# Kernel tuning notes

Hardware: AMD Instinct MI355X
Metric: run time of the kernel (lower is better)

## Reference

```python
import jax, jax.numpy as jnp
import numpy as np

B, S, HID = 1, 2048, 4096
NH, NKV, D = 32, 8, 128
SCALE = D ** -0.5


def _rope_tables(seq_len, head_dim, base=10000.0):
    inv_freq = 1.0 / (base ** (jnp.arange(0, head_dim, 2, dtype=jnp.float32) / head_dim))
    freqs = jnp.arange(seq_len, dtype=jnp.float32)[:, None] * inv_freq[None, :]  # [S, D/2]
    emb = jnp.concatenate([freqs, freqs], axis=-1)  # [S, D]
    return jnp.cos(emb), jnp.sin(emb)


def _rotate_half(x):
    half = x.shape[-1] // 2
    return jnp.concatenate([-x[..., half:], x[..., :half]], axis=-1)


def setup_inputs() -> dict:
    key = jax.random.key(0)
    ks = jax.random.split(key, 5)
    hidden = jax.random.normal(ks[0], (B, S, HID), dtype=jnp.float32)
    cos, sin = _rope_tables(S, D)
    # additive causal mask: 0 on/below diagonal, large negative above
    neg = jnp.full((S, S), -1e9, dtype=jnp.float32)
    causal_mask = jnp.triu(neg, k=1)[None, None]  # [1,1,S,S]
    std_in = HID ** -0.5
    Wq = jax.random.normal(ks[1], (HID, NH * D), dtype=jnp.float32) * std_in
    Wk = jax.random.normal(ks[2], (HID, NKV * D), dtype=jnp.float32) * std_in
    Wv = jax.random.normal(ks[3], (HID, NKV * D), dtype=jnp.float32) * std_in
    Wo = jax.random.normal(ks[4], (NH * D, HID), dtype=jnp.float32) * ((NH * D) ** -0.5)
    return {"hidden": hidden, "cos": cos, "sin": sin, "causal_mask": causal_mask,
            "Wq": Wq, "Wk": Wk, "Wv": Wv, "Wo": Wo}


def reference(hidden, cos, sin, causal_mask, Wq, Wk, Wv, Wo):
    b, s, _ = hidden.shape
    q = (hidden @ Wq).reshape(b, s, NH, D).transpose(0, 2, 1, 3)    # [B,H,S,D]
    k = (hidden @ Wk).reshape(b, s, NKV, D).transpose(0, 2, 1, 3)   # [B,Hkv,S,D]
    v = (hidden @ Wv).reshape(b, s, NKV, D).transpose(0, 2, 1, 3)
    c = cos[None, None]  # [1,1,S,D]
    sn = sin[None, None]
    q = q * c + _rotate_half(q) * sn
    k = k * c + _rotate_half(k) * sn
    group = NH // NKV
    if group > 1:
        k = jnp.repeat(k, group, axis=1)  # [B,H,S,D]
        v = jnp.repeat(v, group, axis=1)
    scores = jnp.einsum('bhsd,bhtd->bhst', q, k) * SCALE + causal_mask
    attn = jax.nn.softmax(scores.astype(jnp.float32), axis=-1).astype(v.dtype)
    ctx = jnp.einsum('bhst,bhtd->bhsd', attn, v)
    ctx = ctx.transpose(0, 2, 1, 3).reshape(b, s, NH * D)
    return ctx @ Wo
```

## Files before the change

### kernel.cpp

```cpp
#include <hip/hip_runtime.h>
#include <hip/hip_bf16.h>
#include <cstdint>
#include <cstddef>

typedef __attribute__((ext_vector_type(8))) short bf16x8;
typedef __attribute__((ext_vector_type(4))) float f32x4;
typedef __attribute__((ext_vector_type(4))) unsigned int u32x4;

__device__ __forceinline__ unsigned short f2bf(float f) {
  __hip_bfloat16 h = __float2bfloat16(f);
  return *reinterpret_cast<unsigned short*>(&h);
}
__device__ __forceinline__ float bf2f(unsigned short u) {
  __hip_bfloat16 h = *reinterpret_cast<__hip_bfloat16*>(&u);
  return __bfloat162float(h);
}

typedef const __attribute__((address_space(1))) void gas_void;
typedef __attribute__((address_space(3))) void las_void;
__device__ __forceinline__ void gload_lds16(const void* g, void* l) {
  __builtin_amdgcn_global_load_lds((gas_void*)g, (las_void*)l, 16, 0, 0);
}

template <int N>
__device__ __forceinline__ void waitcnt_vm() {
  asm volatile("s_waitcnt vmcnt(%0)" :: "i"(N) : "memory");
}
#define LGKM0 { asm volatile("s_waitcnt lgkmcnt(0)" ::: "memory"); \
                __builtin_amdgcn_sched_barrier(0); }

#define S_LEN 2048
#define HID 4096
#define NH 32
#define NKV 8
#define HD 128
#define NQKV 6144
static const float ATT_SCALE = 0.08838834764831845f;


__global__ void prep_kernel(const float* __restrict__ hidden, short* __restrict__ hid_bf,
                            const float* __restrict__ Wq, const float* __restrict__ Wk,
                            const float* __restrict__ Wv, const float* __restrict__ Wo,
                            short* __restrict__ Wcat, short* __restrict__ WoT) {
  __shared__ float tile[64][33];
  const int bid = blockIdx.x;
  const int t = threadIdx.x;
  if (bid >= 20480) {
    int i = ((bid - 20480) * 256 + t) * 8;
    f32x4 a = *(const f32x4*)(hidden + i);
    f32x4 b = *(const f32x4*)(hidden + i + 4);
    unsigned short o[8];
#pragma unroll
    for (int k = 0; k < 4; ++k) { o[k] = f2bf(a[k]); o[4 + k] = f2bf(b[k]); }
    *(u32x4*)(hid_bf + i) = *(const u32x4*)o;
    return;
  }
  const float* src; short* dst; int N, loc;
  if (bid < 8192)       { src = Wq; dst = Wcat;                      N = 4096; loc = bid; }
  else if (bid < 10240) { src = Wk; dst = Wcat + (size_t)4096 * HID; N = 1024; loc = bid - 8192; }
  else if (bid < 12288) { src = Wv; dst = Wcat + (size_t)5120 * HID; N = 1024; loc = bid - 10240; }
  else                  { src = Wo; dst = WoT;                       N = 4096; loc = bid - 12288; }
  const int kb = (loc & 63) * 64, nb = (loc >> 6) * 32;
  {
    int kr = t >> 3, c4 = (t & 7) * 4;
#pragma unroll
    for (int i = 0; i < 2; ++i) {
      int k = kr + i * 32;
      f32x4 v = *(const f32x4*)(src + (size_t)(kb + k) * N + nb + c4);
      tile[k][c4] = v[0]; tile[k][c4 + 1] = v[1];
      tile[k][c4 + 2] = v[2]; tile[k][c4 + 3] = v[3];
    }
  }
  __syncthreads();
  int n = t >> 3, k0 = (t & 7) * 8;
  unsigned short o[8];
#pragma unroll
  for (int i = 0; i < 8; ++i) o[i] = f2bf(tile[k0 + i][n]);
  *(u32x4*)(dst + (size_t)(nb + n) * HID + kb + k0) = *(const u32x4*)o;
}


#define READ_A(MHL) { \
    const short* As_ = lds + (kt & 1) * BUF; \
    _Pragma("unroll") for (int m = 0; m < MHALF; ++m) \
    _Pragma("unroll") for (int kk = 0; kk < 2; ++kk) { \
      int row = (MHL) * (BM / 2) + wr * MSTEP + m * 16 + r; \
      int c = kk * 4 + g; \
      af[m][kk] = *(const bf16x8*)(As_ + row * 64 + ((c ^ (row & 7)) * 8)); \
    } }
#define READ_B(NHL) { \
    const short* Bs_ = lds + (kt & 1) * BUF + BM * 64; \
    _Pragma("unroll") for (int n = 0; n < NHALF; ++n) \
    _Pragma("unroll") for (int kk = 0; kk < 2; ++kk) { \
      int row = (NHL) * (BN / 2) + wc * NSTEP + n * 16 + r; \
      int c = kk * 4 + g; \
      bf[n][kk] = *(const bf16x8*)(Bs_ + row * 64 + ((c ^ (row & 7)) * 8)); \
    } }
#define MFMA_QUAD(MHL, NHL) { \
    __builtin_amdgcn_s_setprio(1); \
    _Pragma("unroll") for (int m = 0; m < MHALF; ++m) \
    _Pragma("unroll") for (int n = 0; n < NHALF; ++n) \
    _Pragma("unroll") for (int kk = 0; kk < 2; ++kk) \
      acc[(MHL)*MHALF + m][(NHL)*NHALF + n] = __builtin_amdgcn_mfma_f32_16x16x32_bf16( \
          af[m][kk], bf[n][kk], acc[(MHL)*MHALF + m][(NHL)*NHALF + n], 0, 0, 0); \
    __builtin_amdgcn_s_setprio(0); }

template <int MODE, int BM, int BN, int WM, int WN>
__global__ __launch_bounds__(WM * WN * 64, 2) void gemm8p_kernel(
    const short* __restrict__ A, const short* __restrict__ Bt,
    int M, int N, int K,
    float* __restrict__ Cf, short* __restrict__ qb_,
    short* __restrict__ kb_, short* __restrict__ vb_) {
  constexpr int NT = WM * WN * 64;
  constexpr int M_FR = BM / (WM * 16);
  constexpr int N_FR = BN / (WN * 16);
  constexpr int MHALF = M_FR / 2;
  constexpr int NHALF = N_FR / 2;
  constexpr int MSTEP = BM / (2 * WM);
  constexpr int NSTEP = BN / (2 * WN);
  constexpr int LA = (BM / 2) * 8 / NT;
  constexpr int LB = (BN / 2) * 8 / NT;
  constexpr int BUF = (BM + BN) * 64;

  __shared__ short lds[2 * BUF];

  const int tid = threadIdx.x, wid = tid >> 6, lane = tid & 63;
  const int wr = wid / WN, wc = wid % WN;
  const int r = lane & 15, g = lane >> 4;
  const int brow = blockIdx.y * BM, bcol = blockIdx.x * BN;
  const int T = K >> 6;

  f32x4 acc[M_FR][N_FR] = {};
  bf16x8 af[MHALF][2], bf[NHALF][2];

  auto stage_rgn = [&](int kt, int rgn) {
    short* buf = lds + (kt & 1) * BUF;
    if (rgn == 0 || rgn == 3) {
      const int mh = (rgn == 3);
      short* dst = buf + mh * (BM / 2) * 64;
      const short* src = A + (size_t)(brow + mh * (BM / 2)) * K + kt * 64;
#pragma unroll
      for (int i = 0; i < LA; ++i) {
        int slot = i * NT + tid;
        int row = slot >> 3, c2 = slot & 7;
        gload_lds16(src + (size_t)row * K + ((c2 ^ (row & 7)) * 8), dst + slot * 8);
      }
    } else {
      const int nh = (rgn == 2);
      short* dst = buf + BM * 64 + nh * (BN / 2) * 64;
      const short* src = Bt + (size_t)(bcol + nh * (BN / 2)) * K + kt * 64;
#pragma unroll
      for (int i = 0; i < LB; ++i) {
        int slot = i * NT + tid;
        int row = slot >> 3, c2 = slot & 7;
        gload_lds16(src + (size_t)row * K + ((c2 ^ (row & 7)) * 8), dst + slot * 8);
      }
    }
  };

  stage_rgn(0, 0); stage_rgn(0, 1); stage_rgn(0, 2); stage_rgn(0, 3);

  for (int kt = 0; kt < T; ++kt) {
    const bool nl = (kt + 1 < T);
    waitcnt_vm<0>();
    __builtin_amdgcn_s_barrier();
    __builtin_amdgcn_sched_barrier(0);
    READ_A(0); READ_B(0);
    if (nl) { stage_rgn(kt + 1, 0); stage_rgn(kt + 1, 1);
              stage_rgn(kt + 1, 2); stage_rgn(kt + 1, 3); }
    LGKM0;
    MFMA_QUAD(0, 0);
    READ_B(1);
    LGKM0;
    MFMA_QUAD(0, 1);
    READ_A(1);
    LGKM0;
    MFMA_QUAD(1, 1);
    READ_B(0);
    LGKM0;
    MFMA_QUAD(1, 0);
  }

  if (MODE == 0) {
#pragma unroll
    for (int fm = 0; fm < M_FR; ++fm)
#pragma unroll
      for (int fn = 0; fn < N_FR; ++fn)
#pragma unroll
        for (int j = 0; j < 4; ++j) {
          int row = brow + (fm / MHALF) * (BM / 2) + wr * MSTEP + (fm % MHALF) * 16 + g * 4 + j;
          int col = bcol + (fn / NHALF) * (BN / 2) + wc * NSTEP + (fn % NHALF) * 16 + r;
          Cf[(size_t)row * N + col] = acc[fm][fn][j];
        }
  } else {
#pragma unroll
    for (int fn = 0; fn < N_FR; ++fn) {
      const int cb = bcol + (fn / NHALF) * (BN / 2) + wc * NSTEP + (fn % NHALF) * 16;
      if (cb < 4096) {
        unsigned short* dst = (unsigned short*)qb_ + (size_t)(cb >> 7) * S_LEN * HD;
        const int d0 = cb & 127;
#pragma unroll
        for (int fm = 0; fm < M_FR; ++fm)
#pragma unroll
          for (int j = 0; j < 4; ++j) {
            int row = brow + (fm / MHALF) * (BM / 2) + wr * MSTEP + (fm % MHALF) * 16 + g * 4 + j;
            dst[(size_t)row * HD + d0 + r] = f2bf(acc[fm][fn][j]);
          }
      } else if (cb < 5120) {
        char* base = (char*)kb_ + ((size_t)((cb - 4096) >> 7) << 19);
        const int d = cb & 127;
#pragma unroll
        for (int fm = 0; fm < M_FR; ++fm)
#pragma unroll
          for (int j = 0; j < 4; ++j) {
            int row = brow + (fm / MHALF) * (BM / 2) + wr * MSTEP + (fm % MHALF) * 16 + g * 4 + j;
            int dd = d + r;
            int krow = row & 63;
            size_t off = ((size_t)(row >> 6) << 14) +
                         ((((krow << 8) + ((dd >> 3) << 4)) ^ ((krow & 7) << 4)) + ((dd & 7) << 1));
            *(unsigned short*)(base + off) = f2bf(acc[fm][fn][j]);
          }
      } else {
        char* base = (char*)vb_ + ((size_t)((cb - 5120) >> 7) << 19);
        const int d = cb & 127;
#pragma unroll
        for (int fm = 0; fm < M_FR; ++fm)
#pragma unroll
          for (int j = 0; j < 4; ++j) {
            int row = brow + (fm / MHALF) * (BM / 2) + wr * MSTEP + (fm % MHALF) * 16 + g * 4 + j;
            int dd = d + r;
            int sl = row & 63;
            size_t off = ((size_t)(row >> 6) << 14) +
                         ((((dd << 7) + ((sl >> 3) << 4)) ^ ((dd & 7) << 4)) + ((sl & 7) << 1));
            *(unsigned short*)(base + off) = f2bf(acc[fm][fn][j]);
          }
      }
    }
  }
}

__global__ void rope_kernel(short* __restrict__ qbuf, short* __restrict__ kbuf,
                            const float* __restrict__ cosT, const float* __restrict__ sinT) {
  int idx = blockIdx.x * 256 + threadIdx.x;
  const int total = (NH + NKV) * S_LEN * 64;
  if (idx >= total) return;
  int d = idx & 63;
  int rowi = idx >> 6;
  int s;
  unsigned short *p1, *p2;
  if (rowi < NH * S_LEN) {
    unsigned short* base = (unsigned short*)qbuf + (size_t)rowi * HD;
    s = rowi & (S_LEN - 1);
    p1 = base + d; p2 = base + d + 64;
  } else {
    int kr = rowi - NH * S_LEN;
    int kvh = kr >> 11; s = kr & (S_LEN - 1);
    char* base = (char*)kbuf + ((size_t)kvh << 19) + ((size_t)(s >> 6) << 14);
    int krow = s & 63, swz = (krow & 7) << 4;
    int dd = d + 64;
    p1 = (unsigned short*)(base + ((((krow << 8) + ((d >> 3) << 4)) ^ swz) + ((d & 7) << 1)));
    p2 = (unsigned short*)(base + ((((krow << 8) + ((dd >> 3) << 4)) ^ swz) + ((dd & 7) << 1)));
  }
  float x1 = bf2f(*p1);
  float x2 = bf2f(*p2);
  float c1 = cosT[s * HD + d], s1 = sinT[s * HD + d];
  *p1 = f2bf(x1 * c1 - x2 * s1);
  *p2 = f2bf(x2 * c1 + x1 * s1);
}

__global__ __launch_bounds__(512, 2) void attn_kernel(const short* __restrict__ qb_,
                                                      const short* __restrict__ kb_,
                                                      const short* __restrict__ vb_,
                                                      short* __restrict__ ctx) {
  const int bid = blockIdx.x;
  const int kvh = bid & 7;
  const int idx = bid >> 3;
  const int h = kvh * 4 + (idx & 3);
  const int slot = idx >> 2;
  const int tid = threadIdx.x, wid = tid >> 6, lane = tid & 63;
  const int r = lane & 15, g = lane >> 4;

  __shared__ short Ks[2][64 * 128];
  __shared__ short Vts[2][128 * 64];
  __shared__ short Ps[8][16 * 64];

  const int qb2s[2] = { slot, 15 - slot };
  const int nt0 = 2 * qb2s[0] + 2;
  const int T = 34;

  const char* kvbase_k = (const char*)kb_ + ((size_t)kvh << 19);
  const char* kvbase_v = (const char*)vb_ + ((size_t)kvh << 19);

  auto stage = [&](int tg, int b) {
    int kvt = (tg < nt0) ? tg : (tg - nt0);
    const char* kt = kvbase_k + ((size_t)kvt << 14);
    const char* vt = kvbase_v + ((size_t)kvt << 14);
#pragma unroll
    for (int i = 0; i < 2; ++i) {
      int ch = i * 8 + wid;
      gload_lds16(kt + ch * 1024 + lane * 16, (char*)&Ks[b][0] + ch * 1024);
      gload_lds16(vt + ch * 1024 + lane * 16, (char*)&Vts[b][0] + ch * 1024);
    }
  };

  stage(0, 0);
  int cur = 0, tglob = 0;

  for (int sec = 0; sec < 2; ++sec) {
    const int qb2 = qb2s[sec];
    const int nt = 2 * qb2 + 2;
    const int rowbase = qb2 * 128 + wid * 16;

    const unsigned short* qptr =
        (const unsigned short*)qb_ + ((size_t)h * S_LEN + rowbase) * HD;
    bf16x8 qf[4];
#pragma unroll
    for (int s4 = 0; s4 < 4; ++s4)
      qf[s4] = *(const bf16x8*)(qptr + (size_t)r * HD + s4 * 32 + g * 8);

    f32x4 oacc[8] = {};
    float m_run[4], l_run[4];
#pragma unroll
    for (int j = 0; j < 4; ++j) { m_run[j] = -1e30f; l_run[j] = 0.f; }

    for (int kvt = 0; kvt < nt; ++kvt, ++tglob) {
      __syncthreads();
      if (tglob + 1 < T) stage(tglob + 1, cur ^ 1);

      const char* Kc = (const char*)&Ks[cur][0];
      const char* Vc = (const char*)&Vts[cur][0];

      f32x4 sv[4] = {};
      __builtin_amdgcn_s_setprio(1);
#pragma unroll
      for (int n = 0; n < 4; ++n) {
        int krow = n * 16 + r;
        int swz = (krow & 7) << 4;
#pragma unroll
        for (int s4 = 0; s4 < 4; ++s4) {
          bf16x8 kf = *(const bf16x8*)(Kc + ((krow * 256 + s4 * 64 + g * 16) ^ swz));
          sv[n] = __builtin_amdgcn_mfma_f32_16x16x32_bf16(qf[s4], kf, sv[n], 0, 0, 0);
        }
      }
      __builtin_amdgcn_s_setprio(0);

      if (kvt * 64 + 63 > rowbase) {
#pragma unroll
        for (int n = 0; n < 4; ++n)
#pragma unroll
          for (int j = 0; j < 4; ++j) {
            int colg = kvt * 64 + n * 16 + r;
            int rowg = rowbase + g * 4 + j;
            sv[n][j] = (colg <= rowg) ? sv[n][j] * ATT_SCALE : -1e30f;
          }
      } else {
#pragma unroll
        for (int n = 0; n < 4; ++n)
#pragma unroll
          for (int j = 0; j < 4; ++j) sv[n][j] *= ATT_SCALE;
      }

      float pmax[4];
#pragma unroll
      for (int j = 0; j < 4; ++j)
        pmax[j] = fmaxf(fmaxf(sv[0][j], sv[1][j]), fmaxf(sv[2][j], sv[3][j]));
#pragma unroll
      for (int msk = 1; msk <= 8; msk <<= 1)
#pragma unroll
        for (int j = 0; j < 4; ++j) pmax[j] = fmaxf(pmax[j], __shfl_xor(pmax[j], msk));

      float sf[4], rsum[4];
#pragma unroll
      for (int j = 0; j < 4; ++j) {
        float mn = fmaxf(m_run[j], pmax[j]);
        sf[j] = __expf(m_run[j] - mn);
        m_run[j] = mn;
        rsum[j] = 0.f;
      }
#pragma unroll
      for (int n = 0; n < 4; ++n)
#pragma unroll
        for (int j = 0; j < 4; ++j) {
          float p = __expf(sv[n][j] - m_run[j]);
          sv[n][j] = p;
          rsum[j] += p;
        }
#pragma unroll
      for (int msk = 1; msk <= 8; msk <<= 1)
#pragma unroll
        for (int j = 0; j < 4; ++j) rsum[j] += __shfl_xor(rsum[j], msk);
#pragma unroll
      for (int j = 0; j < 4; ++j) l_run[j] = l_run[j] * sf[j] + rsum[j];
#pragma unroll
      for (int t = 0; t < 8; ++t)
#pragma unroll
        for (int j = 0; j < 4; ++j) oacc[t][j] *= sf[j];

#pragma unroll
      for (int n = 0; n < 4; ++n)
#pragma unroll
        for (int j = 0; j < 4; ++j) {
          int prow = g * 4 + j, pcol = n * 16 + r;
          int poff = (prow * 128 + pcol * 2) ^ ((prow & 7) << 4);
          *(unsigned short*)((char*)&Ps[wid][0] + poff) = f2bf(sv[n][j]);
        }

      __builtin_amdgcn_s_setprio(1);
#pragma unroll
      for (int s4 = 0; s4 < 2; ++s4) {
        bf16x8 pf = *(const bf16x8*)((const char*)&Ps[wid][0] +
                                     ((r * 128 + s4 * 64 + g * 16) ^ ((r & 7) << 4)));
#pragma unroll
        for (int t = 0; t < 8; ++t) {
          int vrow = t * 16 + r;
          bf16x8 vf = *(const bf16x8*)(Vc + ((vrow * 128 + s4 * 64 + g * 16) ^ ((vrow & 7) << 4)));
          oacc[t] = __builtin_amdgcn_mfma_f32_16x16x32_bf16(pf, vf, oacc[t], 0, 0, 0);
        }
      }
      __builtin_amdgcn_s_setprio(0);
      cur ^= 1;
    }

    float inv[4];
#pragma unroll
    for (int j = 0; j < 4; ++j) inv[j] = 1.0f / l_run[j];
#pragma unroll
    for (int t = 0; t < 8; ++t)
#pragma unroll
      for (int j = 0; j < 4; ++j) {
        int rowg = rowbase + g * 4 + j;
        int colg = h * HD + t * 16 + r;
        ((unsigned short*)ctx)[(size_t)rowg * HID + colg] = f2bf(oacc[t][j] * inv[j]);
      }
  }
}

extern "C" void kernel_launch(void* const* d_in, const int* in_sizes, int n_in,
                              void* d_out, int out_size, void* d_ws, size_t ws_size,
                              hipStream_t stream) {
  const float* hidden = (const float*)d_in[0];
  const float* cosT   = (const float*)d_in[1];
  const float* sinT   = (const float*)d_in[2];
  const float* Wq = (const float*)d_in[4];
  const float* Wk = (const float*)d_in[5];
  const float* Wv = (const float*)d_in[6];
  const float* Wo = (const float*)d_in[7];
  float* out = (float*)d_out;

  char* ws = (char*)d_ws;
  short* hid_bf = (short*)(ws);
  short* Wcat   = (short*)(ws + 16777216);
  short* WoT    = (short*)(ws + 67108864);
  short* qbuf   = (short*)(ws + 100663296);
  short* kbuf   = (short*)(ws + 117440512);
  short* vbuf   = (short*)(ws + 121634816);
  short* ctx    = (short*)(ws + 125829120);

  prep_kernel<<<24576, 256, 0, stream>>>(hidden, hid_bf, Wq, Wk, Wv, Wo, Wcat, WoT);

  gemm8p_kernel<1, 128, 384, 2, 4><<<dim3(16, 16), 512, 0, stream>>>(
      hid_bf, Wcat, S_LEN, NQKV, HID, nullptr, qbuf, kbuf, vbuf);

  rope_kernel<<<20480, 256, 0, stream>>>(qbuf, kbuf, cosT, sinT);

  attn_kernel<<<256, 512, 0, stream>>>(qbuf, kbuf, vbuf, ctx);

  gemm8p_kernel<0, 128, 256, 2, 4><<<dim3(16, 16), 512, 0, stream>>>(
      ctx, WoT, S_LEN, HID, HID, out, nullptr, nullptr, nullptr);
}
```

Before: 320.0 us.

## Fuse Q RoPE into attention, shrink GEMM tiles, unify staging loop

Q rotary embedding now runs inside the attention kernel on the register-resident Q fragments, so the rope kernel only touches K. This removes a full read-modify-write pass over the Q buffer. Both GEMMs move to smaller tiles (128x192 and 128x128) with a 4x2 warp layout and twice as many blocks, which raises parallelism across CUs but lowers per-block data reuse. The global-to-LDS staging is merged into a single loop over A and B rows.

```diff
diff --git a/kernel.cpp b/kernel.cpp
--- a/kernel.cpp
+++ b/kernel.cpp
@@ -26,8 +26,6 @@
 __device__ __forceinline__ void waitcnt_vm() {
   asm volatile("s_waitcnt vmcnt(%0)" :: "i"(N) : "memory");
 }
-#define LGKM0 { asm volatile("s_waitcnt lgkmcnt(0)" ::: "memory"); \
-                __builtin_amdgcn_sched_barrier(0); }
 
 #define S_LEN 2048
 #define HID 4096
@@ -106,20 +104,18 @@
     __builtin_amdgcn_s_setprio(0); }
 
 template <int MODE, int BM, int BN, int WM, int WN>
-__global__ __launch_bounds__(WM * WN * 64, 2) void gemm8p_kernel(
+__global__ __launch_bounds__(512, 2) void gemmms_kernel(
     const short* __restrict__ A, const short* __restrict__ Bt,
     int M, int N, int K,
     float* __restrict__ Cf, short* __restrict__ qb_,
     short* __restrict__ kb_, short* __restrict__ vb_) {
-  constexpr int NT = WM * WN * 64;
   constexpr int M_FR = BM / (WM * 16);
   constexpr int N_FR = BN / (WN * 16);
   constexpr int MHALF = M_FR / 2;
   constexpr int NHALF = N_FR / 2;
   constexpr int MSTEP = BM / (2 * WM);
   constexpr int NSTEP = BN / (2 * WN);
-  constexpr int LA = (BM / 2) * 8 / NT;
-  constexpr int LB = (BN / 2) * 8 / NT;
+  constexpr int LT = (BM + BN) * 8 / 512;
   constexpr int BUF = (BM + BN) * 64;
 
   __shared__ short lds[2 * BUF];
@@ -133,32 +129,20 @@
   f32x4 acc[M_FR][N_FR] = {};
   bf16x8 af[MHALF][2], bf[NHALF][2];
 
-  auto stage_rgn = [&](int kt, int rgn) {
+  auto stage = [&](int kt) {
     short* buf = lds + (kt & 1) * BUF;
-    if (rgn == 0 || rgn == 3) {
-      const int mh = (rgn == 3);
-      short* dst = buf + mh * (BM / 2) * 64;
-      const short* src = A + (size_t)(brow + mh * (BM / 2)) * K + kt * 64;
-#pragma unroll
-      for (int i = 0; i < LA; ++i) {
-        int slot = i * NT + tid;
-        int row = slot >> 3, c2 = slot & 7;
-        gload_lds16(src + (size_t)row * K + ((c2 ^ (row & 7)) * 8), dst + slot * 8);
-      }
-    } else {
-      const int nh = (rgn == 2);
-      short* dst = buf + BM * 64 + nh * (BN / 2) * 64;
-      const short* src = Bt + (size_t)(bcol + nh * (BN / 2)) * K + kt * 64;
-#pragma unroll
-      for (int i = 0; i < LB; ++i) {
-        int slot = i * NT + tid;
-        int row = slot >> 3, c2 = slot & 7;
-        gload_lds16(src + (size_t)row * K + ((c2 ^ (row & 7)) * 8), dst + slot * 8);
-      }
+#pragma unroll
+    for (int i = 0; i < LT; ++i) {
+      int slot = i * 512 + tid;
+      int row = slot >> 3, c2 = slot & 7;
+      const short* src = (row < BM)
+          ? A + (size_t)(brow + row) * K + kt * 64 + ((c2 ^ (row & 7)) * 8)
+          : Bt + (size_t)(bcol + row - BM) * K + kt * 64 + ((c2 ^ (row & 7)) * 8);
+      gload_lds16(src, buf + slot * 8);
     }
   };
 
-  stage_rgn(0, 0); stage_rgn(0, 1); stage_rgn(0, 2); stage_rgn(0, 3);
+  stage(0);
 
   for (int kt = 0; kt < T; ++kt) {
     const bool nl = (kt + 1 < T);
@@ -166,18 +150,21 @@
     __builtin_amdgcn_s_barrier();
     __builtin_amdgcn_sched_barrier(0);
     READ_A(0); READ_B(0);
-    if (nl) { stage_rgn(kt + 1, 0); stage_rgn(kt + 1, 1);
-              stage_rgn(kt + 1, 2); stage_rgn(kt + 1, 3); }
-    LGKM0;
+    if (nl) stage(kt + 1);
+    asm volatile("s_waitcnt lgkmcnt(0)" ::: "memory");
+    __builtin_amdgcn_sched_barrier(0);
     MFMA_QUAD(0, 0);
     READ_B(1);
-    LGKM0;
+    asm volatile("s_waitcnt lgkmcnt(0)" ::: "memory");
+    __builtin_amdgcn_sched_barrier(0);
     MFMA_QUAD(0, 1);
     READ_A(1);
-    LGKM0;
+    asm volatile("s_waitcnt lgkmcnt(0)" ::: "memory");
+    __builtin_amdgcn_sched_barrier(0);
     MFMA_QUAD(1, 1);
     READ_B(0);
-    LGKM0;
+    asm volatile("s_waitcnt lgkmcnt(0)" ::: "memory");
+    __builtin_amdgcn_sched_barrier(0);
     MFMA_QUAD(1, 0);
   }
 
@@ -239,28 +226,19 @@
   }
 }
 
-__global__ void rope_kernel(short* __restrict__ qbuf, short* __restrict__ kbuf,
+__global__ void rope_kernel(short* __restrict__ kbuf,
                             const float* __restrict__ cosT, const float* __restrict__ sinT) {
   int idx = blockIdx.x * 256 + threadIdx.x;
-  const int total = (NH + NKV) * S_LEN * 64;
+  const int total = NKV * S_LEN * 64;
   if (idx >= total) return;
   int d = idx & 63;
-  int rowi = idx >> 6;
-  int s;
-  unsigned short *p1, *p2;
-  if (rowi < NH * S_LEN) {
-    unsigned short* base = (unsigned short*)qbuf + (size_t)rowi * HD;
-    s = rowi & (S_LEN - 1);
-    p1 = base + d; p2 = base + d + 64;
-  } else {
-    int kr = rowi - NH * S_LEN;
-    int kvh = kr >> 11; s = kr & (S_LEN - 1);
-    char* base = (char*)kbuf + ((size_t)kvh << 19) + ((size_t)(s >> 6) << 14);
-    int krow = s & 63, swz = (krow & 7) << 4;
-    int dd = d + 64;
-    p1 = (unsigned short*)(base + ((((krow << 8) + ((d >> 3) << 4)) ^ swz) + ((d & 7) << 1)));
-    p2 = (unsigned short*)(base + ((((krow << 8) + ((dd >> 3) << 4)) ^ swz) + ((dd & 7) << 1)));
-  }
+  int kr = idx >> 6;
+  int kvh = kr >> 11, s = kr & (S_LEN - 1);
+  char* base = (char*)kbuf + ((size_t)kvh << 19) + ((size_t)(s >> 6) << 14);
+  int krow = s & 63, swz = (krow & 7) << 4;
+  int dd = d + 64;
+  unsigned short* p1 = (unsigned short*)(base + ((((krow << 8) + ((d >> 3) << 4)) ^ swz) + ((d & 7) << 1)));
+  unsigned short* p2 = (unsigned short*)(base + ((((krow << 8) + ((dd >> 3) << 4)) ^ swz) + ((dd & 7) << 1)));
   float x1 = bf2f(*p1);
   float x2 = bf2f(*p2);
   float c1 = cosT[s * HD + d], s1 = sinT[s * HD + d];
@@ -271,7 +249,9 @@
 __global__ __launch_bounds__(512, 2) void attn_kernel(const short* __restrict__ qb_,
                                                       const short* __restrict__ kb_,
                                                       const short* __restrict__ vb_,
-                                                      short* __restrict__ ctx) {
+                                                      short* __restrict__ ctx,
+                                                      const float* __restrict__ cosT,
+                                                      const float* __restrict__ sinT) {
   const int bid = blockIdx.x;
   const int kvh = bid & 7;
   const int idx = bid >> 3;
@@ -317,6 +297,28 @@
 #pragma unroll
     for (int s4 = 0; s4 < 4; ++s4)
       qf[s4] = *(const bf16x8*)(qptr + (size_t)r * HD + s4 * 32 + g * 8);
+
+    {
+      const int s = rowbase + r;
+      const float* cp = cosT + (size_t)s * HD + g * 8;
+      const float* sp = sinT + (size_t)s * HD + g * 8;
+#pragma unroll
+      for (int s4 = 0; s4 < 2; ++s4) {
+        f32x4 c0 = *(const f32x4*)(cp + s4 * 32);
+        f32x4 c1 = *(const f32x4*)(cp + s4 * 32 + 4);
+        f32x4 sn0 = *(const f32x4*)(sp + s4 * 32);
+        f32x4 sn1 = *(const f32x4*)(sp + s4 * 32 + 4);
+#pragma unroll
+        for (int j = 0; j < 8; ++j) {
+          float cc = (j < 4) ? c0[j & 3] : c1[j & 3];
+          float ss = (j < 4) ? sn0[j & 3] : sn1[j & 3];
+          float x1 = bf2f((unsigned short)qf[s4][j]);
+          float x2 = bf2f((unsigned short)qf[s4 + 2][j]);
+          qf[s4][j] = (short)f2bf(x1 * cc - x2 * ss);
+          qf[s4 + 2][j] = (short)f2bf(x2 * cc + x1 * ss);
+        }
+      }
+    }
 
     f32x4 oacc[8] = {};
     float m_run[4], l_run[4];
@@ -458,13 +460,13 @@
 
   prep_kernel<<<24576, 256, 0, stream>>>(hidden, hid_bf, Wq, Wk, Wv, Wo, Wcat, WoT);
 
-  gemm8p_kernel<1, 128, 384, 2, 4><<<dim3(16, 16), 512, 0, stream>>>(
+  gemmms_kernel<1, 128, 192, 4, 2><<<dim3(32, 16), 512, 0, stream>>>(
       hid_bf, Wcat, S_LEN, NQKV, HID, nullptr, qbuf, kbuf, vbuf);
 
-  rope_kernel<<<20480, 256, 0, stream>>>(qbuf, kbuf, cosT, sinT);
-
-  attn_kernel<<<256, 512, 0, stream>>>(qbuf, kbuf, vbuf, ctx);
-
-  gemm8p_kernel<0, 128, 256, 2, 4><<<dim3(16, 16), 512, 0, stream>>>(
+  rope_kernel<<<4096, 256, 0, stream>>>(kbuf, cosT, sinT);
+
+  attn_kernel<<<256, 512, 0, stream>>>(qbuf, kbuf, vbuf, ctx, cosT, sinT);
+
+  gemmms_kernel<0, 128, 128, 4, 2><<<dim3(32, 16), 512, 0, stream>>>(
       ctx, WoT, S_LEN, HID, HID, out, nullptr, nullptr, nullptr);
 }
```

New measurement: 322.1 us. No clear change (+0.7%).
